# Kernel tuning notes

Measured on AMD Instinct MI355X. Metric: run time of the kernel, lower is better.

The kernel has to match this reference:

```python
import jax, jax.numpy as jnp
import numpy as np

B, TV, TS, D = 16, 256, 32, 512


def setup_inputs() -> dict:
    key = jax.random.key(0)
    ks = jax.random.split(key, 8)
    return {
        "video_feature": jax.random.normal(ks[0], (B, TV, D), dtype=jnp.float32),
        "video_mask": jnp.ones((B, TV), dtype=jnp.float32),
        "sentence_feature": jax.random.normal(ks[1], (B, TS, D), dtype=jnp.float32),
        "sentence_mask": jnp.ones((B, TS), dtype=jnp.float32),
        "w1": jax.random.normal(ks[2], (D, D), dtype=jnp.float32) * (1.0 / np.sqrt(D)),
        "b1": jax.random.normal(ks[3], (D,), dtype=jnp.float32) * 0.02,
        "w2": jax.random.normal(ks[4], (D, D), dtype=jnp.float32) * (1.0 / np.sqrt(D)),
        "wt": jax.random.normal(ks[5], (D,), dtype=jnp.float32) * (1.0 / np.sqrt(D)),
    }


def reference(video_feature, video_mask, sentence_feature, sentence_mask, w1, b1, w2, wt):
    # tmp1: [B, Tv, D] masked video projection (Linear with bias)
    tmp1 = (jnp.einsum("bvd,ed->bve", video_feature, w1) + b1) * video_mask[:, :, None]
    # tmp2: [B, Ts, D] masked sentence projection (Linear, no bias)
    tmp2 = jnp.einsum("bsd,ed->bse", sentence_feature, w2) * sentence_mask[:, :, None]
    # pairwise mask: [B, Tv, Ts]
    pair_mask = video_mask[:, :, None] * sentence_mask[:, None, :]
    # broadcast-add -> [B, Tv, Ts, D], mask, tanh, reduce with wt -> [B, Tv, Ts]
    tmp = (tmp1[:, :, None, :] + tmp2[:, None, :, :]) * pair_mask[..., None]
    M = jnp.einsum("bvsd,d->bvs", jnp.tanh(tmp), wt)
    return M * pair_mask
```

## Files before the change

kernel.cpp:

```cpp
#include <hip/hip_runtime.h>

#define BB 16
#define TV 256
#define TS 32
#define DD 512

typedef float    floatx4  __attribute__((ext_vector_type(4)));
typedef short    short8   __attribute__((ext_vector_type(8)));
typedef unsigned short ushort8 __attribute__((ext_vector_type(8)));

#define TANH_SCALE 2.885390082f

static __device__ __forceinline__ unsigned short f2bf(float f) {
    unsigned int u = __float_as_uint(f);
    u += 0x7FFFu + ((u >> 16) & 1u);
    return (unsigned short)(u >> 16);
}

__global__ __launch_bounds__(256) void ta_convert(
    const float* __restrict__ video, const float* __restrict__ sent,
    const float* __restrict__ w1,    const float* __restrict__ w2,
    unsigned short* __restrict__ vb, unsigned short* __restrict__ sb,
    unsigned short* __restrict__ w1b, unsigned short* __restrict__ w2b)
{
    const int NV = BB * TV * DD, NS = BB * TS * DD, NW = DD * DD;
    const int base = (blockIdx.x * 256 + threadIdx.x) * 8;
    const float* src; unsigned short* dst; int off;
    if      (base < NV)           { src = video; dst = vb;  off = base; }
    else if (base < NV + NS)      { src = sent;  dst = sb;  off = base - NV; }
    else if (base < NV + NS + NW) { src = w1;    dst = w1b; off = base - NV - NS; }
    else                          { src = w2;    dst = w2b; off = base - NV - NS - NW; }
    const float4 a = *(const float4*)(src + off);
    const float4 b = *(const float4*)(src + off + 4);
    ushort8 o;
    o[0] = f2bf(a.x); o[1] = f2bf(a.y); o[2] = f2bf(a.z); o[3] = f2bf(a.w);
    o[4] = f2bf(b.x); o[5] = f2bf(b.y); o[6] = f2bf(b.z); o[7] = f2bf(b.w);
    *(ushort8*)(dst + off) = o;
}

__global__ __launch_bounds__(256) void ta_mfma_gemm(
    const unsigned short* __restrict__ vb, const unsigned short* __restrict__ w1b,
    const float* __restrict__ b1,          const float* __restrict__ vmask,
    unsigned short* __restrict__ tmp1h,
    const unsigned short* __restrict__ sb, const unsigned short* __restrict__ w2b,
    const float* __restrict__ smask,       unsigned short* __restrict__ tmp2h,
    const float* __restrict__ wt,          float* __restrict__ wsum)
{
    const int t = threadIdx.x;

    if (blockIdx.x == 0 && t < 64) {
        float v = 0.f;
        for (int i = t; i < DD; i += 64) v += wt[i];
        for (int off = 32; off; off >>= 1) v += __shfl_down(v, off);
        if (t == 0) wsum[0] = v;
    }

    const bool g2 = (blockIdx.x >= 512);
    const int bid = g2 ? (int)blockIdx.x - 512 : (int)blockIdx.x;
    const unsigned short* __restrict__ A = g2 ? sb    : vb;
    const unsigned short* __restrict__ W = g2 ? w2b   : w1b;
    const float* __restrict__ rm         = g2 ? smask : vmask;
    const int m0 = (g2 ? (bid & 7)  : (bid & 63)) * 64;
    const int n0 = (g2 ? (bid >> 3) : (bid >> 6)) * 64;

    __shared__ unsigned short As[2][4096];
    __shared__ unsigned short Bs[2][4096];

    const int lane = t & 63;
    const int wid  = t >> 6;
    const int wm   = wid >> 1, wn = wid & 1;
    const int lr   = lane & 15, kg = lane >> 4;

    const int r0 = t >> 3,          g0c = (t & 7) ^ (r0 & 7);
    const int r1 = (t + 256) >> 3,  g1c = (t & 7) ^ (r1 & 7);
    const unsigned short* a0p = A + (size_t)(m0 + r0) * DD + g0c * 8;
    const unsigned short* a1p = A + (size_t)(m0 + r1) * DD + g1c * 8;
    const unsigned short* w0p = W + (size_t)(n0 + r0) * DD + g0c * 8;
    const unsigned short* w1p = W + (size_t)(n0 + r1) * DD + g1c * 8;
    const int l0 = t * 8;
    const int l1 = (t + 256) * 8;

#define TA_STAGE(buf, koff) do {                                               \
    __builtin_amdgcn_global_load_lds(                                          \
        (const __attribute__((address_space(1))) void*)(a0p + (koff)),         \
        (__attribute__((address_space(3))) void*)&As[buf][l0], 16, 0, 0);      \
    __builtin_amdgcn_global_load_lds(                                          \
        (const __attribute__((address_space(1))) void*)(a1p + (koff)),         \
        (__attribute__((address_space(3))) void*)&As[buf][l1], 16, 0, 0);      \
    __builtin_amdgcn_global_load_lds(                                          \
        (const __attribute__((address_space(1))) void*)(w0p + (koff)),         \
        (__attribute__((address_space(3))) void*)&Bs[buf][l0], 16, 0, 0);      \
    __builtin_amdgcn_global_load_lds(                                          \
        (const __attribute__((address_space(1))) void*)(w1p + (koff)),         \
        (__attribute__((address_space(3))) void*)&Bs[buf][l1], 16, 0, 0);      \
  } while (0)

    floatx4 acc[2][2] = {};

    const int ml0 = wm * 32 + lr, ml1 = ml0 + 16;
    const int nl0 = wn * 32 + lr, nl1 = nl0 + 16;
    const int sa0 = ml0 * 64, sa1 = ml1 * 64;
    const int sb0 = nl0 * 64, sb1 = nl1 * 64;
    const int xa = ml0 & 7, xb = nl0 & 7;

    TA_STAGE(0, 0);
    __syncthreads();

    int cur = 0;
    for (int step = 0; step < 8; ++step) {
        if (step < 7) TA_STAGE(cur ^ 1, (step + 1) * 64);
#pragma unroll
        for (int kk = 0; kk < 2; ++kk) {
            const int kc = kk * 4 + kg;
            short8 a0 = *(const short8*)&As[cur][sa0 + ((kc ^ xa) << 3)];
            short8 a1 = *(const short8*)&As[cur][sa1 + ((kc ^ xa) << 3)];
            short8 b0 = *(const short8*)&Bs[cur][sb0 + ((kc ^ xb) << 3)];
            short8 b1 = *(const short8*)&Bs[cur][sb1 + ((kc ^ xb) << 3)];
            acc[0][0] = __builtin_amdgcn_mfma_f32_16x16x32_bf16(a0, b0, acc[0][0], 0, 0, 0);
            acc[0][1] = __builtin_amdgcn_mfma_f32_16x16x32_bf16(a0, b1, acc[0][1], 0, 0, 0);
            acc[1][0] = __builtin_amdgcn_mfma_f32_16x16x32_bf16(a1, b0, acc[1][0], 0, 0, 0);
            acc[1][1] = __builtin_amdgcn_mfma_f32_16x16x32_bf16(a1, b1, acc[1][1], 0, 0, 0);
        }
        __syncthreads();
        cur ^= 1;
    }
#undef TA_STAGE

#pragma unroll
    for (int fm = 0; fm < 2; ++fm)
#pragma unroll
        for (int fn = 0; fn < 2; ++fn)
#pragma unroll
            for (int r = 0; r < 4; ++r) {
                const int m = m0 + wm * 32 + fm * 16 + kg * 4 + r;
                const int n = n0 + wn * 32 + fn * 16 + lr;
                const float mk = rm[m] * TANH_SCALE;
                float z = g2 ? (acc[fm][fn][r] * mk)
                             : (acc[fm][fn][r] + b1[n]) * mk;
                z = fminf(fmaxf(z, -30.f), 30.f);
                const float e = __builtin_amdgcn_exp2f(z);
                if (!g2) {
                    tmp1h[(size_t)m * DD + n] = f2bf(e);
                } else {
                    const int bb = m >> 5, ss = m & 31;
                    tmp2h[(size_t)bb * 16384 + (size_t)(ss >> 4) * 8192
                          + (size_t)(n >> 1) * 32 + (ss & 15) * 2 + (n & 1)] = f2bf(e);
                }
            }
}

__global__ __launch_bounds__(256, 6) void ta_tanh_main(
    const unsigned short* __restrict__ tmp1h,
    const unsigned short* __restrict__ tmp2h,
    const float* __restrict__ wt,
    const float* __restrict__ wsum,
    const float* __restrict__ vmask,
    const float* __restrict__ smask,
    float* __restrict__ out)
{
    __shared__ unsigned int   e2u[4096];
    __shared__ unsigned short e1u[4 * 520];
    __shared__ float part[512];

    const int t   = threadIdx.x;
    const int bid = blockIdx.x;
    const int b   = bid >> 7;
    const int vt  = (bid >> 1) & 63;
    const int sh  = bid & 1;
    const int v0  = vt << 2;

    {
        const unsigned short* e2src = tmp2h + (size_t)b * 16384 + sh * 8192 + t * 8;
#pragma unroll
        for (int i = 0; i < 4; ++i) {
            __builtin_amdgcn_global_load_lds(
                (const __attribute__((address_space(1))) void*)(e2src + i * 2048),
                (__attribute__((address_space(3))) void*)&e2u[t * 4 + i * 1024], 16, 0, 0);
        }
        const int row = t >> 6, col = (t & 63) * 8;
        __builtin_amdgcn_global_load_lds(
            (const __attribute__((address_space(1))) void*)
                (tmp1h + (size_t)(b * TV + v0 + row) * DD + col),
            (__attribute__((address_space(3))) void*)&e1u[row * 520 + col], 16, 0, 0);
    }
    __syncthreads();

    const int s  = t & 15;
    const int vi = (t >> 4) & 1;
    const int q  = t >> 5;

    const unsigned short* __restrict__ e1lo = e1u + vi * 520 + q * 64;
    const unsigned short* __restrict__ e1hi = e1u + (vi + 2) * 520 + q * 64;
    const float* __restrict__ wtp = wt + q * 64;
    const int ubase = q * 512 + s;

    floatx4 alo = {0.f, 0.f, 0.f, 0.f};
    floatx4 ahi = {0.f, 0.f, 0.f, 0.f};
#pragma unroll
    for (int i = 0; i < 8; ++i) {
        const int ub = ubase + i * 64;
        const unsigned u0 = e2u[ub];
        const unsigned u1 = e2u[ub + 16];
        const unsigned u2 = e2u[ub + 32];
        const unsigned u3 = e2u[ub + 48];
        ushort8 l8 = *(const ushort8*)(e1lo + i * 8);
        ushort8 h8 = *(const ushort8*)(e1hi + i * 8);
        floatx4 wa = *(const floatx4*)(wtp + i * 8);
        floatx4 wb = *(const floatx4*)(wtp + i * 8 + 4);
        const float e2v[8] = {
            __uint_as_float(u0 << 16), __uint_as_float(u0 & 0xffff0000u),
            __uint_as_float(u1 << 16), __uint_as_float(u1 & 0xffff0000u),
            __uint_as_float(u2 << 16), __uint_as_float(u2 & 0xffff0000u),
            __uint_as_float(u3 << 16), __uint_as_float(u3 & 0xffff0000u)
        };
#pragma unroll
        for (int j = 0; j < 4; ++j) {
            const float xl = __uint_as_float((unsigned)l8[j] << 16);
            const float xh = __uint_as_float((unsigned)h8[j] << 16);
            const float rl = __builtin_amdgcn_rcpf(fmaf(xl, e2v[j], 1.f));
            const float rh = __builtin_amdgcn_rcpf(fmaf(xh, e2v[j], 1.f));
            alo[j] = fmaf(wa[j], rl, alo[j]);
            ahi[j] = fmaf(wa[j], rh, ahi[j]);
        }
#pragma unroll
        for (int j = 0; j < 4; ++j) {
            const float xl = __uint_as_float((unsigned)l8[j + 4] << 16);
            const float xh = __uint_as_float((unsigned)h8[j + 4] << 16);
            const float rl = __builtin_amdgcn_rcpf(fmaf(xl, e2v[j + 4], 1.f));
            const float rh = __builtin_amdgcn_rcpf(fmaf(xh, e2v[j + 4], 1.f));
            alo[j] = fmaf(wb[j], rl, alo[j]);
            ahi[j] = fmaf(wb[j], rh, ahi[j]);
        }
    }

    part[(vi    ) * 128 + s * 8 + q] = (alo[0] + alo[1]) + (alo[2] + alo[3]);
    part[(vi + 2) * 128 + s * 8 + q] = (ahi[0] + ahi[1]) + (ahi[2] + ahi[3]);
    __syncthreads();

    if (t < 64) {
        const int vrow = t >> 4, s2 = t & 15;
        const floatx4 p0 = *(const floatx4*)&part[vrow * 128 + s2 * 8];
        const floatx4 p1 = *(const floatx4*)&part[vrow * 128 + s2 * 8 + 4];
        const float sum = ((p0[0] + p0[1]) + (p0[2] + p0[3]))
                        + ((p1[0] + p1[1]) + (p1[2] + p1[3]));
        const int v  = v0 + vrow;
        const int sg = sh * 16 + s2;
        const float pm = vmask[b * TV + v] * smask[b * TS + sg];
        out[((size_t)b * TV + v) * TS + sg] = pm * (wsum[0] - 2.f * sum);
    }
}

extern "C" void kernel_launch(void* const* d_in, const int* in_sizes, int n_in,
                              void* d_out, int out_size, void* d_ws, size_t ws_size,
                              hipStream_t stream)
{
    const float* video = (const float*)d_in[0];
    const float* vmask = (const float*)d_in[1];
    const float* sent  = (const float*)d_in[2];
    const float* smask = (const float*)d_in[3];
    const float* w1    = (const float*)d_in[4];
    const float* b1    = (const float*)d_in[5];
    const float* w2    = (const float*)d_in[6];
    const float* wt    = (const float*)d_in[7];
    float* out = (float*)d_out;

    const size_t NV = (size_t)BB * TV * DD, NS = (size_t)BB * TS * DD, NW = (size_t)DD * DD;

    unsigned short* tmp1h = (unsigned short*)d_ws;
    unsigned short* tmp2h = tmp1h + NV;
    unsigned short* vb    = tmp2h + NS;
    unsigned short* sb    = vb + NV;
    unsigned short* w1b   = sb + NS;
    unsigned short* w2b   = w1b + NW;
    float* wsum           = (float*)(w2b + NW);

    const int total8 = (int)((NV + NS + 2 * NW) / 8);
    ta_convert<<<dim3(total8 / 256), dim3(256), 0, stream>>>(
        video, sent, w1, w2, vb, sb, w1b, w2b);
    ta_mfma_gemm<<<dim3(512 + 64), dim3(256), 0, stream>>>(
        vb, w1b, b1, vmask, tmp1h, sb, w2b, smask, tmp2h, wt, wsum);
    ta_tanh_main<<<dim3(BB * (TV / 4) * 2), dim3(256), 0, stream>>>(
        tmp1h, tmp2h, wt, wsum, vmask, smask, out);
}
```

Before: 35.28 us.

## Process 16 video rows per block in tanh kernel to reuse staged sentence tile

Each block of the pairwise tanh kernel now handles 16 video rows instead of 4, so the 16 KB tmp2 tile loaded into LDS is reused four times as much, and the grid shrinks from 2048 to 512 blocks. Each thread keeps four accumulators across video rows and loops over 128 of the d dimension instead of 64, and the final reduction is done by all threads over 4 partials. This cuts redundant tmp2 loads and per-block setup, at the cost of more LDS and registers per block and fewer blocks for latency hiding. The occupancy hint on launch bounds is removed.

```diff
diff --git a/kernel.cpp b/kernel.cpp
--- a/kernel.cpp
+++ b/kernel.cpp
@@ -47,14 +47,12 @@
     const float* __restrict__ wt,          float* __restrict__ wsum)
 {
     const int t = threadIdx.x;
-
     if (blockIdx.x == 0 && t < 64) {
         float v = 0.f;
         for (int i = t; i < DD; i += 64) v += wt[i];
         for (int off = 32; off; off >>= 1) v += __shfl_down(v, off);
         if (t == 0) wsum[0] = v;
     }
-
     const bool g2 = (blockIdx.x >= 512);
     const int bid = g2 ? (int)blockIdx.x - 512 : (int)blockIdx.x;
     const unsigned short* __restrict__ A = g2 ? sb    : vb;
@@ -96,7 +94,6 @@
   } while (0)
 
     floatx4 acc[2][2] = {};
-
     const int ml0 = wm * 32 + lr, ml1 = ml0 + 16;
     const int nl0 = wn * 32 + lr, nl1 = nl0 + 16;
     const int sa0 = ml0 * 64, sa1 = ml1 * 64;
@@ -105,7 +102,6 @@
 
     TA_STAGE(0, 0);
     __syncthreads();
-
     int cur = 0;
     for (int step = 0; step < 8; ++step) {
         if (step < 7) TA_STAGE(cur ^ 1, (step + 1) * 64);
@@ -149,7 +145,7 @@
             }
 }
 
-__global__ __launch_bounds__(256, 6) void ta_tanh_main(
+__global__ __launch_bounds__(256) void ta_tanh_main(
     const unsigned short* __restrict__ tmp1h,
     const unsigned short* __restrict__ tmp2h,
     const float* __restrict__ wt,
@@ -159,15 +155,14 @@
     float* __restrict__ out)
 {
     __shared__ unsigned int   e2u[4096];
-    __shared__ unsigned short e1u[4 * 520];
-    __shared__ float part[512];
+    __shared__ unsigned short e1u[16 * 520];
+    __shared__ float part[1024];
 
     const int t   = threadIdx.x;
     const int bid = blockIdx.x;
-    const int b   = bid >> 7;
-    const int vt  = (bid >> 1) & 63;
-    const int sh  = bid & 1;
-    const int v0  = vt << 2;
+    const int b   = bid >> 5;
+    const int sh  = (bid >> 4) & 1;
+    const int v0  = (bid & 15) << 4;
 
     {
         const unsigned short* e2src = tmp2h + (size_t)b * 16384 + sh * 8192 + t * 8;
@@ -177,34 +172,41 @@
                 (const __attribute__((address_space(1))) void*)(e2src + i * 2048),
                 (__attribute__((address_space(3))) void*)&e2u[t * 4 + i * 1024], 16, 0, 0);
         }
-        const int row = t >> 6, col = (t & 63) * 8;
-        __builtin_amdgcn_global_load_lds(
-            (const __attribute__((address_space(1))) void*)
-                (tmp1h + (size_t)(b * TV + v0 + row) * DD + col),
-            (__attribute__((address_space(3))) void*)&e1u[row * 520 + col], 16, 0, 0);
+#pragma unroll
+        for (int i = 0; i < 4; ++i) {
+            const int c = t + 256 * i;
+            const int row = c >> 6, col = (c & 63) * 8;
+            __builtin_amdgcn_global_load_lds(
+                (const __attribute__((address_space(1))) void*)
+                    (tmp1h + (size_t)(b * TV + v0 + row) * DD + col),
+                (__attribute__((address_space(3))) void*)&e1u[row * 520 + col], 16, 0, 0);
+        }
     }
     __syncthreads();
 
     const int s  = t & 15;
-    const int vi = (t >> 4) & 1;
-    const int q  = t >> 5;
-
-    const unsigned short* __restrict__ e1lo = e1u + vi * 520 + q * 64;
-    const unsigned short* __restrict__ e1hi = e1u + (vi + 2) * 520 + q * 64;
-    const float* __restrict__ wtp = wt + q * 64;
-    const int ubase = q * 512 + s;
-
-    floatx4 alo = {0.f, 0.f, 0.f, 0.f};
-    floatx4 ahi = {0.f, 0.f, 0.f, 0.f};
-#pragma unroll
-    for (int i = 0; i < 8; ++i) {
-        const int ub = ubase + i * 64;
+    const int vi = (t >> 4) & 3;
+    const int q  = t >> 6;
+
+    const float* __restrict__ wtp = wt + q * 128;
+    const int d2b = q * 64;
+
+    floatx4 acc0 = {0.f, 0.f, 0.f, 0.f};
+    floatx4 acc1 = {0.f, 0.f, 0.f, 0.f};
+    floatx4 acc2 = {0.f, 0.f, 0.f, 0.f};
+    floatx4 acc3 = {0.f, 0.f, 0.f, 0.f};
+#pragma unroll 4
+    for (int i = 0; i < 16; ++i) {
+        const int ub = (d2b + i * 4) * 16 + s;
         const unsigned u0 = e2u[ub];
         const unsigned u1 = e2u[ub + 16];
         const unsigned u2 = e2u[ub + 32];
         const unsigned u3 = e2u[ub + 48];
-        ushort8 l8 = *(const ushort8*)(e1lo + i * 8);
-        ushort8 h8 = *(const ushort8*)(e1hi + i * 8);
+        const int e1off = q * 128 + i * 8;
+        ushort8 r0 = *(const ushort8*)(e1u + (vi     ) * 520 + e1off);
+        ushort8 r1 = *(const ushort8*)(e1u + (vi +  4) * 520 + e1off);
+        ushort8 r2 = *(const ushort8*)(e1u + (vi +  8) * 520 + e1off);
+        ushort8 r3 = *(const ushort8*)(e1u + (vi + 12) * 520 + e1off);
         floatx4 wa = *(const floatx4*)(wtp + i * 8);
         floatx4 wb = *(const floatx4*)(wtp + i * 8 + 4);
         const float e2v[8] = {
@@ -215,34 +217,38 @@
         };
 #pragma unroll
         for (int j = 0; j < 4; ++j) {
-            const float xl = __uint_as_float((unsigned)l8[j] << 16);
-            const float xh = __uint_as_float((unsigned)h8[j] << 16);
-            const float rl = __builtin_amdgcn_rcpf(fmaf(xl, e2v[j], 1.f));
-            const float rh = __builtin_amdgcn_rcpf(fmaf(xh, e2v[j], 1.f));
-            alo[j] = fmaf(wa[j], rl, alo[j]);
-            ahi[j] = fmaf(wa[j], rh, ahi[j]);
+            const float x0 = __uint_as_float((unsigned)r0[j] << 16);
+            const float x1 = __uint_as_float((unsigned)r1[j] << 16);
+            const float x2 = __uint_as_float((unsigned)r2[j] << 16);
+            const float x3 = __uint_as_float((unsigned)r3[j] << 16);
+            acc0[j] = fmaf(wa[j], __builtin_amdgcn_rcpf(fmaf(x0, e2v[j], 1.f)), acc0[j]);
+            acc1[j] = fmaf(wa[j], __builtin_amdgcn_rcpf(fmaf(x1, e2v[j], 1.f)), acc1[j]);
+            acc2[j] = fmaf(wa[j], __builtin_amdgcn_rcpf(fmaf(x2, e2v[j], 1.f)), acc2[j]);
+            acc3[j] = fmaf(wa[j], __builtin_amdgcn_rcpf(fmaf(x3, e2v[j], 1.f)), acc3[j]);
         }
 #pragma unroll
         for (int j = 0; j < 4; ++j) {
-            const float xl = __uint_as_float((unsigned)l8[j + 4] << 16);
-            const float xh = __uint_as_float((unsigned)h8[j + 4] << 16);
-            const float rl = __builtin_amdgcn_rcpf(fmaf(xl, e2v[j + 4], 1.f));
-            const float rh = __builtin_amdgcn_rcpf(fmaf(xh, e2v[j + 4], 1.f));
-            alo[j] = fmaf(wb[j], rl, alo[j]);
-            ahi[j] = fmaf(wb[j], rh, ahi[j]);
-        }
-    }
-
-    part[(vi    ) * 128 + s * 8 + q] = (alo[0] + alo[1]) + (alo[2] + alo[3]);
-    part[(vi + 2) * 128 + s * 8 + q] = (ahi[0] + ahi[1]) + (ahi[2] + ahi[3]);
+            const float x0 = __uint_as_float((unsigned)r0[j + 4] << 16);
+            const float x1 = __uint_as_float((unsigned)r1[j + 4] << 16);
+            const float x2 = __uint_as_float((unsigned)r2[j + 4] << 16);
+            const float x3 = __uint_as_float((unsigned)r3[j + 4] << 16);
+            acc0[j] = fmaf(wb[j], __builtin_amdgcn_rcpf(fmaf(x0, e2v[j + 4], 1.f)), acc0[j]);
+            acc1[j] = fmaf(wb[j], __builtin_amdgcn_rcpf(fmaf(x1, e2v[j + 4], 1.f)), acc1[j]);
+            acc2[j] = fmaf(wb[j], __builtin_amdgcn_rcpf(fmaf(x2, e2v[j + 4], 1.f)), acc2[j]);
+            acc3[j] = fmaf(wb[j], __builtin_amdgcn_rcpf(fmaf(x3, e2v[j + 4], 1.f)), acc3[j]);
+        }
+    }
+
+    part[(vi     ) * 64 + s * 4 + q] = (acc0[0] + acc0[1]) + (acc0[2] + acc0[3]);
+    part[(vi +  4) * 64 + s * 4 + q] = (acc1[0] + acc1[1]) + (acc1[2] + acc1[3]);
+    part[(vi +  8) * 64 + s * 4 + q] = (acc2[0] + acc2[1]) + (acc2[2] + acc2[3]);
+    part[(vi + 12) * 64 + s * 4 + q] = (acc3[0] + acc3[1]) + (acc3[2] + acc3[3]);
     __syncthreads();
 
-    if (t < 64) {
+    {
         const int vrow = t >> 4, s2 = t & 15;
-        const floatx4 p0 = *(const floatx4*)&part[vrow * 128 + s2 * 8];
-        const floatx4 p1 = *(const floatx4*)&part[vrow * 128 + s2 * 8 + 4];
-        const float sum = ((p0[0] + p0[1]) + (p0[2] + p0[3]))
-                        + ((p1[0] + p1[1]) + (p1[2] + p1[3]));
+        const floatx4 p = *(const floatx4*)&part[vrow * 64 + s2 * 4];
+        const float sum = (p[0] + p[1]) + (p[2] + p[3]);
         const int v  = v0 + vrow;
         const int sg = sh * 16 + s2;
         const float pm = vmask[b * TV + v] * smask[b * TS + sg];
@@ -279,6 +285,6 @@
         video, sent, w1, w2, vb, sb, w1b, w2b);
     ta_mfma_gemm<<<dim3(512 + 64), dim3(256), 0, stream>>>(
         vb, w1b, b1, vmask, tmp1h, sb, w2b, smask, tmp2h, wt, wsum);
-    ta_tanh_main<<<dim3(BB * (TV / 4) * 2), dim3(256), 0, stream>>>(
+    ta_tanh_main<<<dim3(512), dim3(256), 0, stream>>>(
         tmp1h, tmp2h, wt, wsum, vmask, smask, out);
 }
```

Measured after the change: 35.41 us. About the same (+0.4%).
